# Optimization experiments

Hardware: AMD Instinct MI355X
Metric: run time of the kernel (lower is better)

Reference implementation:

```python
import jax, jax.numpy as jnp
import numpy as np

N, T, D, P, NB = 32768, 128, 32, 16, 15


def setup_inputs() -> dict:
    key = jax.random.key(0)
    ks = jax.random.split(key, 8)
    S = jax.random.normal(ks[0], (N, T, 1), dtype=jnp.float32)
    L_dyn = jax.random.normal(ks[1], (N, T, D), dtype=jnp.float32)
    C_static = jax.random.normal(ks[2], (N, P), dtype=jnp.float32)
    Y = jax.random.randint(ks[3], (N, T, 1), 0, 2).astype(jnp.float32)
    mask = jnp.ones((N, T), dtype=jnp.float32)
    return {
        "S": S, "L_dyn": L_dyn, "C_static": C_static, "Y": Y, "mask": mask,
        "psi": jnp.array([0.5], jnp.float32),
        "gamma_A": jnp.array([0.1], jnp.float32),
        "w_gamma_dyn": 0.05 * jax.random.normal(ks[4], (D,), dtype=jnp.float32),
        "w_gamma_static": 0.05 * jax.random.normal(ks[5], (P,), dtype=jnp.float32),
        "log_sigma_Z": jnp.array([-0.5], jnp.float32),
        "beta_0": jnp.array([-4.0], jnp.float32),
        "beta_Z": jnp.array([0.3], jnp.float32),
        "beta_bins": jnp.zeros((NB,), jnp.float32),
        "w_beta_dyn": 0.1 * jax.random.normal(ks[6], (D,), dtype=jnp.float32),
        "w_beta_static": 0.1 * jax.random.normal(ks[7], (P,), dtype=jnp.float32),
        "beta_time": jnp.array([0.03], jnp.float32),
    }


def reference(S, L_dyn, C_static, Y, mask, psi, gamma_A, w_gamma_dyn,
              w_gamma_static, log_sigma_Z, beta_0, beta_Z, beta_bins,
              w_beta_dyn, w_beta_static, beta_time):
    n, t_len = S.shape[0], S.shape[1]
    nb = beta_bins.shape[0]
    edges = jnp.linspace(-2.5, 2.5, nb + 1).astype(S.dtype)
    # torch.bucketize(s, edges[1:-1]) (right=False) == searchsorted side='left'
    idx = jnp.clip(jnp.searchsorted(edges[1:-1], S[..., 0], side='left'), 0, nb - 1)
    bin_eff = beta_bins[idx][..., None]            # (N,T,1) == (A_bin * beta_bins).sum(-1)
    sigma_sq = jnp.exp(log_sigma_Z)[0] ** 2        # sigma_Z^2
    gd = L_dyn @ w_gamma_dyn[:, None]              # (N,T,1) gamma_dyn(L)
    bd = L_dyn @ w_beta_dyn[:, None]               # (N,T,1) beta_dyn(L)
    gs = (C_static @ w_gamma_static)[:, None]      # (N,1) gamma_static(C)
    bs = (C_static @ w_beta_static)[:, None]       # (N,1) beta_static(C)
    tt = jnp.arange(t_len, dtype=S.dtype) / 30.0   # beta_time * (t/30)

    xs = (
        jnp.swapaxes(S, 0, 1),        # (T,N,1)
        jnp.swapaxes(gd, 0, 1),
        jnp.swapaxes(bd, 0, 1),
        jnp.swapaxes(bin_eff, 0, 1),
        jnp.swapaxes(Y, 0, 1),
        mask.T[:, :, None],           # (T,N,1)
        tt,
    )
    psi_s, gA, bZ, b0, bT = psi[0], gamma_A[0], beta_Z[0], beta_0[0], beta_time[0]

    def step(carry, x):
        Z_mean, Z_var, ll = carry
        A_t, gd_t, bd_t, be_t, Y_t, m_t, t_s = x
        # latent transition prior
        Z_pred_mean = psi_s * Z_mean + gA * A_t + gd_t + gs
        Z_pred_var = psi_s ** 2 * Z_var + sigma_sq
        # outcome probability
        logit = b0 + bZ * Z_pred_mean + be_t + bd_t + bs + bT * t_s
        prob = jax.nn.sigmoid(jnp.clip(logit, -20.0, 20.0))
        # approximate Kalman (Laplace) update from Y
        grad = (Y_t - prob) * bZ * m_t
        hess = bZ ** 2 * prob * (1.0 - prob) * m_t + 1e-6
        Z_post_var = 1.0 / (1.0 / (Z_pred_var + 1e-8) + hess)
        Z_post_mean = Z_pred_mean + Z_post_var * grad
        ll_t = ((Y_t * jnp.log(prob + 1e-10)
                 + (1.0 - Y_t) * jnp.log(1.0 - prob + 1e-10)) * m_t).sum()
        return (Z_post_mean, Z_post_var, ll + ll_t), (Z_post_mean, Z_post_var)

    init = (jnp.zeros((n, 1), S.dtype), jnp.ones((n, 1), S.dtype),
            jnp.zeros((), S.dtype))
    (_, _, ll), (Zf, Zv) = jax.lax.scan(step, init, xs)
    return jnp.swapaxes(Zf, 0, 1), jnp.swapaxes(Zv, 0, 1), ll
```

## Files before the change

kernel.cpp:

```cpp
#include <hip/hip_runtime.h>

#define T_LEN 128
#define NB_BINS 15

__global__ __launch_bounds__(256) void k_static(
    const float4* __restrict__ C4,
    const float4* __restrict__ wgs4,
    const float4* __restrict__ wbs4,
    float* __restrict__ gs_out, float* __restrict__ bs_out, int n_seq)
{
    int n = blockIdx.x * blockDim.x + threadIdx.x;
    if (n >= n_seq) return;
    float gs = 0.0f, bs = 0.0f;
    #pragma unroll
    for (int i = 0; i < 4; ++i) {
        float4 c = C4[n * 4 + i];
        float4 wg = wgs4[i];
        float4 wb = wbs4[i];
        gs += c.x * wg.x + c.y * wg.y + c.z * wg.z + c.w * wg.w;
        bs += c.x * wb.x + c.y * wb.y + c.z * wb.z + c.w * wb.w;
    }
    gs_out[n] = gs;
    bs_out[n] = bs;
}

__global__ __launch_bounds__(256) void k_pre(
    const float4* __restrict__ L4,
    const float*  __restrict__ S,
    const float*  __restrict__ gs_in,
    const float*  __restrict__ bs_in,
    const float4* __restrict__ wgd4,
    const float4* __restrict__ wbd4,
    const float*  __restrict__ p_gA,
    const float*  __restrict__ p_b0,
    const float*  __restrict__ p_bbins,
    const float*  __restrict__ p_bT,
    float* __restrict__ a_out,
    float* __restrict__ c_out,
    int total_rows)
{
    __shared__ float sbins[NB_BINS];
    if (threadIdx.x < NB_BINS) sbins[threadIdx.x] = p_bbins[threadIdx.x];
    __syncthreads();

    const float gA   = p_gA[0];
    const float b0   = p_b0[0];
    const float bT30 = p_bT[0] * (1.0f / 30.0f);

    const int tid   = blockIdx.x * blockDim.x + threadIdx.x;
    const int lane8 = tid & 7;
    const float4 wg = wgd4[lane8];
    const float4 wb = wbd4[lane8];

    const int group   = tid >> 3;
    const int ngroups = (gridDim.x * blockDim.x) >> 3;

    int row = group;
    float4 v = (row < total_rows) ? L4[(size_t)row * 8 + lane8]
                                  : make_float4(0, 0, 0, 0);
    for (; row < total_rows; row += ngroups) {
        const int nrow = row + ngroups;
        float4 vn = v;
        if (nrow < total_rows) vn = L4[(size_t)nrow * 8 + lane8];

        float g = v.x * wg.x + v.y * wg.y + v.z * wg.z + v.w * wg.w;
        float b = v.x * wb.x + v.y * wb.y + v.z * wb.z + v.w * wb.w;
        #pragma unroll
        for (int off = 1; off < 8; off <<= 1) {
            g += __shfl_xor(g, off, 64);
            b += __shfl_xor(b, off, 64);
        }

        const int n = row >> 7;
        const int t = row & 127;
        const float s_v = S[row];
        const float gsv = gs_in[n];
        const float bsv = bs_in[n];
        int cnt = (int)fmaxf(0.0f, fminf(14.0f,
                      ceilf(fmaf(s_v, 3.0f, 7.5f)) - 1.0f));
        const float a = gA * s_v + g + gsv;
        const float c = b0 + sbins[cnt] + b + bsv + bT30 * (float)t;

        if (lane8 == 0) { a_out[row] = a; c_out[row] = c; }
        v = vn;
    }
}

__global__ __launch_bounds__(256) void k_scan(
    const float4* Ain,
    const float4* Cin,
    const float4* __restrict__ Y4,
    const float4* __restrict__ M4,
    const float*  __restrict__ p_psi,
    const float*  __restrict__ p_lsz,
    const float*  __restrict__ p_bZ,
    float4* Zf4,
    float4* Zv4,
    float* __restrict__ ll_out)
{
    const int gtid = blockIdx.x * blockDim.x + threadIdx.x;
    const int n = gtid >> 2;
    const int s = gtid & 3;

    const float psi  = p_psi[0];
    const float e    = __expf(p_lsz[0]);
    const float sig2 = e * e;
    const float bZ   = p_bZ[0];
    const float psi2 = psi * psi;
    const float bZ2  = bZ * bZ;

    const int b32 = n * 32;

    float zm = 0.0f, zvv = 1.0f, ll = 0.0f;

#define STEP(AA, CC, YY, MM, PMOUT, PVOUT, PROUT) do {                    \
        const float zpm = fmaf(psi, zm, (AA));                            \
        const float zpv = fmaf(psi2, zvv, sig2);                          \
        float logit = fmaf(bZ, zpm, (CC));                                \
        logit = fminf(fmaxf(logit, -20.0f), 20.0f);                       \
        const float prob = __builtin_amdgcn_rcpf(1.0f + __expf(-logit));  \
        const float grad = ((YY) - prob) * bZ * (MM);                     \
        const float hess = fmaf(bZ2 * prob * (1.0f - prob), (MM), 1e-6f); \
        const float pvv  = __builtin_amdgcn_rcpf(                         \
                             __builtin_amdgcn_rcpf(zpv + 1e-8f) + hess);  \
        const float pmm  = fmaf(pvv, grad, zpm);                          \
        zm = pmm; zvv = pvv;                                              \
        PMOUT = pmm; PVOUT = pvv; PROUT = prob;                           \
    } while (0)

#define CHUNK(J, Aq, Cq, Yq, Mq) do {                                     \
        float pm0, pm1, pm2, pm3, pv0, pv1, pv2, pv3, pr0, pr1, pr2, pr3; \
        STEP(Aq.x, Cq.x, Yq.x, Mq.x, pm0, pv0, pr0);                      \
        STEP(Aq.y, Cq.y, Yq.y, Mq.y, pm1, pv1, pr1);                      \
        STEP(Aq.z, Cq.z, Yq.z, Mq.z, pm2, pv2, pr2);                      \
        STEP(Aq.w, Cq.w, Yq.w, Mq.w, pm3, pv3, pr3);                      \
        const float prs = (s == 0) ? pr0 : (s == 1) ? pr1                 \
                        : (s == 2) ? pr2 : pr3;                           \
        const float ys  = (s == 0) ? Yq.x : (s == 1) ? Yq.y               \
                        : (s == 2) ? Yq.z : Yq.w;                         \
        const float ms  = (s == 0) ? Mq.x : (s == 1) ? Mq.y               \
                        : (s == 2) ? Mq.z : Mq.w;                         \
        ll += (ys * __logf(prs + 1e-10f)                                  \
             + (1.0f - ys) * __logf(1.0f - prs + 1e-10f)) * ms;           \
        if (s == (J)) {                                                   \
            stpm = make_float4(pm0, pm1, pm2, pm3);                       \
            stpv = make_float4(pv0, pv1, pv2, pv3);                       \
        }                                                                 \
    } while (0)

    float4 A0 = Ain[b32 + 0], A1 = Ain[b32 + 1], A2 = Ain[b32 + 2], A3 = Ain[b32 + 3];
    float4 C0 = Cin[b32 + 0], C1 = Cin[b32 + 1], C2 = Cin[b32 + 2], C3 = Cin[b32 + 3];
    float4 Y0 = Y4[b32 + 0],  Y1 = Y4[b32 + 1],  Y2 = Y4[b32 + 2],  Y3 = Y4[b32 + 3];
    float4 M0 = M4[b32 + 0],  M1 = M4[b32 + 1],  M2 = M4[b32 + 2],  M3 = M4[b32 + 3];

    for (int Q = 0; Q < 8; ++Q) {
        float4 An0, An1, An2, An3, Cn0, Cn1, Cn2, Cn3;
        float4 Yn0, Yn1, Yn2, Yn3, Mn0, Mn1, Mn2, Mn3;
        if (Q < 7) {
            const int qb = b32 + 4 * (Q + 1);
            An0 = Ain[qb + 0]; An1 = Ain[qb + 1]; An2 = Ain[qb + 2]; An3 = Ain[qb + 3];
            Cn0 = Cin[qb + 0]; Cn1 = Cin[qb + 1]; Cn2 = Cin[qb + 2]; Cn3 = Cin[qb + 3];
            Yn0 = Y4[qb + 0];  Yn1 = Y4[qb + 1];  Yn2 = Y4[qb + 2];  Yn3 = Y4[qb + 3];
            Mn0 = M4[qb + 0];  Mn1 = M4[qb + 1];  Mn2 = M4[qb + 2];  Mn3 = M4[qb + 3];
        }

        float4 stpm = make_float4(0, 0, 0, 0);
        float4 stpv = make_float4(0, 0, 0, 0);
        CHUNK(0, A0, C0, Y0, M0);
        CHUNK(1, A1, C1, Y1, M1);
        CHUNK(2, A2, C2, Y2, M2);
        CHUNK(3, A3, C3, Y3, M3);

        Zf4[b32 + 4 * Q + s] = stpm;
        Zv4[b32 + 4 * Q + s] = stpv;

        if (Q < 7) {
            A0 = An0; A1 = An1; A2 = An2; A3 = An3;
            C0 = Cn0; C1 = Cn1; C2 = Cn2; C3 = Cn3;
            Y0 = Yn0; Y1 = Yn1; Y2 = Yn2; Y3 = Yn3;
            M0 = Mn0; M1 = Mn1; M2 = Mn2; M3 = Mn3;
        }
    }
#undef CHUNK
#undef STEP

    #pragma unroll
    for (int off = 1; off < 64; off <<= 1) ll += __shfl_xor(ll, off, 64);
    if ((threadIdx.x & 63) == 0) atomicAdd(ll_out, ll);
}

extern "C" void kernel_launch(void* const* d_in, const int* in_sizes, int n_in,
                              void* d_out, int out_size, void* d_ws, size_t ws_size,
                              hipStream_t stream) {
    const float* S     = (const float*)d_in[0];
    const float* L     = (const float*)d_in[1];
    const float* C     = (const float*)d_in[2];
    const float* Y     = (const float*)d_in[3];
    const float* M     = (const float*)d_in[4];
    const float* psi   = (const float*)d_in[5];
    const float* gA    = (const float*)d_in[6];
    const float* wgd   = (const float*)d_in[7];
    const float* wgs   = (const float*)d_in[8];
    const float* lsz   = (const float*)d_in[9];
    const float* b0    = (const float*)d_in[10];
    const float* bZ    = (const float*)d_in[11];
    const float* bbins = (const float*)d_in[12];
    const float* wbd   = (const float*)d_in[13];
    const float* wbs   = (const float*)d_in[14];
    const float* bT    = (const float*)d_in[15];

    const int NT    = in_sizes[0];
    const int n_seq = NT / T_LEN;

    float* zf = (float*)d_out;
    float* zv = zf + NT;
    float* ll = zf + 2 * (size_t)NT;

    float* gs_ws = (float*)d_ws;
    float* bs_ws = gs_ws + n_seq;

    hipMemsetAsync((void*)ll, 0, sizeof(float), stream);

    k_static<<<(n_seq + 255) / 256, 256, 0, stream>>>(
        reinterpret_cast<const float4*>(C),
        reinterpret_cast<const float4*>(wgs),
        reinterpret_cast<const float4*>(wbs),
        gs_ws, bs_ws, n_seq);

    k_pre<<<2048, 256, 0, stream>>>(
        reinterpret_cast<const float4*>(L),
        S, gs_ws, bs_ws,
        reinterpret_cast<const float4*>(wgd),
        reinterpret_cast<const float4*>(wbd),
        gA, b0, bbins, bT,
        zf, zv, NT);

    k_scan<<<(n_seq * 4) / 256, 256, 0, stream>>>(
        reinterpret_cast<const float4*>(zf),
        reinterpret_cast<const float4*>(zv),
        reinterpret_cast<const float4*>(Y),
        reinterpret_cast<const float4*>(M),
        psi, lsz, bZ,
        reinterpret_cast<float4*>(zf),
        reinterpret_cast<float4*>(zv),
        ll);
}
```

Measured before the change: 182.2 us.

## Fuse static projection into preprocessing and stage time-major packed inputs for scan

Folds the static-covariate projection into the preprocessing kernel, which now packs (a, c, Y, mask) into one float4 per step. It transposes these through shared memory into a time-major workspace so the scan kernel can do coalesced loads. The scan drops the redundant 4-thread-per-sequence recompute and runs one thread per sequence with triple-buffered prefetch. This removes a launch and the duplicated step work, but the scan's per-thread output writes are strided, and it launches only 64-thread blocks (512 total).

New measurement: 194.7 us. +6.9%, slower.

```diff
diff --git a/kernel.cpp b/kernel.cpp
--- a/kernel.cpp
+++ b/kernel.cpp
@@ -2,66 +2,66 @@
 
 #define T_LEN 128
 #define NB_BINS 15
-
-__global__ __launch_bounds__(256) void k_static(
+#define SEQS_PER_BLOCK 16
+
+__global__ __launch_bounds__(256) void k_pre(
+    const float4* __restrict__ L4,
+    const float*  __restrict__ S,
+    const float*  __restrict__ Y,
+    const float*  __restrict__ M,
     const float4* __restrict__ C4,
     const float4* __restrict__ wgs4,
     const float4* __restrict__ wbs4,
-    float* __restrict__ gs_out, float* __restrict__ bs_out, int n_seq)
-{
-    int n = blockIdx.x * blockDim.x + threadIdx.x;
-    if (n >= n_seq) return;
-    float gs = 0.0f, bs = 0.0f;
-    #pragma unroll
-    for (int i = 0; i < 4; ++i) {
-        float4 c = C4[n * 4 + i];
-        float4 wg = wgs4[i];
-        float4 wb = wbs4[i];
-        gs += c.x * wg.x + c.y * wg.y + c.z * wg.z + c.w * wg.w;
-        bs += c.x * wb.x + c.y * wb.y + c.z * wb.z + c.w * wb.w;
-    }
-    gs_out[n] = gs;
-    bs_out[n] = bs;
-}
-
-__global__ __launch_bounds__(256) void k_pre(
-    const float4* __restrict__ L4,
-    const float*  __restrict__ S,
-    const float*  __restrict__ gs_in,
-    const float*  __restrict__ bs_in,
     const float4* __restrict__ wgd4,
     const float4* __restrict__ wbd4,
     const float*  __restrict__ p_gA,
     const float*  __restrict__ p_b0,
     const float*  __restrict__ p_bbins,
     const float*  __restrict__ p_bT,
-    float* __restrict__ a_out,
-    float* __restrict__ c_out,
-    int total_rows)
+    float4* __restrict__ staged,
+    int Nseq)
 {
+    __shared__ float4 tile[T_LEN][SEQS_PER_BLOCK + 1];
+    __shared__ float sgs[SEQS_PER_BLOCK], sbs[SEQS_PER_BLOCK];
     __shared__ float sbins[NB_BINS];
-    if (threadIdx.x < NB_BINS) sbins[threadIdx.x] = p_bbins[threadIdx.x];
+
+    const int tid = threadIdx.x;
+    if (tid < NB_BINS) sbins[tid] = p_bbins[tid];
+
+    const int n0 = blockIdx.x * SEQS_PER_BLOCK;
+
+    if (tid < SEQS_PER_BLOCK) {
+        float gs = 0.0f, bs = 0.0f;
+        #pragma unroll
+        for (int i = 0; i < 4; ++i) {
+            float4 c  = C4[(n0 + tid) * 4 + i];
+            float4 wg = wgs4[i];
+            float4 wb = wbs4[i];
+            gs += c.x * wg.x + c.y * wg.y + c.z * wg.z + c.w * wg.w;
+            bs += c.x * wb.x + c.y * wb.y + c.z * wb.z + c.w * wb.w;
+        }
+        sgs[tid] = gs; sbs[tid] = bs;
+    }
     __syncthreads();
 
     const float gA   = p_gA[0];
     const float b0   = p_b0[0];
     const float bT30 = p_bT[0] * (1.0f / 30.0f);
 
-    const int tid   = blockIdx.x * blockDim.x + threadIdx.x;
     const int lane8 = tid & 7;
+    const int gid   = tid >> 3;
     const float4 wg = wgd4[lane8];
     const float4 wb = wbd4[lane8];
 
-    const int group   = tid >> 3;
-    const int ngroups = (gridDim.x * blockDim.x) >> 3;
-
-    int row = group;
-    float4 v = (row < total_rows) ? L4[(size_t)row * 8 + lane8]
-                                  : make_float4(0, 0, 0, 0);
-    for (; row < total_rows; row += ngroups) {
-        const int nrow = row + ngroups;
+    const size_t rowbase = (size_t)n0 * T_LEN;
+
+    float4 v = L4[(rowbase + gid) * 8 + lane8];
+    for (int it = 0; it < 64; ++it) {
+        const int    lrow = it * 32 + gid;
+        const size_t row  = rowbase + lrow;
+
         float4 vn = v;
-        if (nrow < total_rows) vn = L4[(size_t)nrow * 8 + lane8];
+        if (it + 1 < 64) vn = L4[(row + 32) * 8 + lane8];
 
         float g = v.x * wg.x + v.y * wg.y + v.z * wg.z + v.w * wg.w;
         float b = v.x * wb.x + v.y * wb.y + v.z * wb.z + v.w * wb.w;
@@ -71,36 +71,40 @@
             b += __shfl_xor(b, off, 64);
         }
 
-        const int n = row >> 7;
-        const int t = row & 127;
+        const int nl = lrow >> 7;
+        const int t  = lrow & 127;
         const float s_v = S[row];
-        const float gsv = gs_in[n];
-        const float bsv = bs_in[n];
+        const float y_v = Y[row];
+        const float m_v = M[row];
         int cnt = (int)fmaxf(0.0f, fminf(14.0f,
                       ceilf(fmaf(s_v, 3.0f, 7.5f)) - 1.0f));
-        const float a = gA * s_v + g + gsv;
-        const float c = b0 + sbins[cnt] + b + bsv + bT30 * (float)t;
-
-        if (lane8 == 0) { a_out[row] = a; c_out[row] = c; }
+        const float a = gA * s_v + g + sgs[nl];
+        const float c = b0 + sbins[cnt] + b + sbs[nl] + bT30 * (float)t;
+
+        if (lane8 == 0) tile[t][nl] = make_float4(a, c, y_v, m_v);
         v = vn;
     }
+    __syncthreads();
+
+    #pragma unroll
+    for (int p = 0; p < 8; ++p) {
+        const int idx = p * 256 + tid;
+        const int t = idx >> 4, j = idx & 15;
+        staged[(size_t)t * Nseq + n0 + j] = tile[t][j];
+    }
 }
 
-__global__ __launch_bounds__(256) void k_scan(
-    const float4* Ain,
-    const float4* Cin,
-    const float4* __restrict__ Y4,
-    const float4* __restrict__ M4,
+__global__ __launch_bounds__(64) void k_scan(
+    const float4* __restrict__ staged,
     const float*  __restrict__ p_psi,
     const float*  __restrict__ p_lsz,
     const float*  __restrict__ p_bZ,
-    float4* Zf4,
-    float4* Zv4,
-    float* __restrict__ ll_out)
+    float4* __restrict__ Zf4,
+    float4* __restrict__ Zv4,
+    float*  __restrict__ ll_out,
+    int Nseq)
 {
-    const int gtid = blockIdx.x * blockDim.x + threadIdx.x;
-    const int n = gtid >> 2;
-    const int s = gtid & 3;
+    const int n = blockIdx.x * 64 + threadIdx.x;
 
     const float psi  = p_psi[0];
     const float e    = __expf(p_lsz[0]);
@@ -109,79 +113,57 @@
     const float psi2 = psi * psi;
     const float bZ2  = bZ * bZ;
 
-    const int b32 = n * 32;
-
     float zm = 0.0f, zvv = 1.0f, ll = 0.0f;
 
-#define STEP(AA, CC, YY, MM, PMOUT, PVOUT, PROUT) do {                    \
-        const float zpm = fmaf(psi, zm, (AA));                            \
+#define STEP(PK, PMOUT, PVOUT) do {                                       \
+        const float zpm = fmaf(psi, zm, PK.x);                            \
         const float zpv = fmaf(psi2, zvv, sig2);                          \
-        float logit = fmaf(bZ, zpm, (CC));                                \
+        float logit = fmaf(bZ, zpm, PK.y);                                \
         logit = fminf(fmaxf(logit, -20.0f), 20.0f);                       \
         const float prob = __builtin_amdgcn_rcpf(1.0f + __expf(-logit));  \
-        const float grad = ((YY) - prob) * bZ * (MM);                     \
-        const float hess = fmaf(bZ2 * prob * (1.0f - prob), (MM), 1e-6f); \
+        const float grad = (PK.z - prob) * bZ * PK.w;                     \
+        const float hess = fmaf(bZ2 * prob * (1.0f - prob), PK.w, 1e-6f); \
         const float pvv  = __builtin_amdgcn_rcpf(                         \
                              __builtin_amdgcn_rcpf(zpv + 1e-8f) + hess);  \
         const float pmm  = fmaf(pvv, grad, zpm);                          \
-        zm = pmm; zvv = pvv;                                              \
-        PMOUT = pmm; PVOUT = pvv; PROUT = prob;                           \
+        ll += (PK.z * __logf(prob + 1e-10f)                               \
+             + (1.0f - PK.z) * __logf(1.0f - prob + 1e-10f)) * PK.w;      \
+        zm = pmm; zvv = pvv; PMOUT = pmm; PVOUT = pvv;                    \
     } while (0)
 
-#define CHUNK(J, Aq, Cq, Yq, Mq) do {                                     \
-        float pm0, pm1, pm2, pm3, pv0, pv1, pv2, pv3, pr0, pr1, pr2, pr3; \
-        STEP(Aq.x, Cq.x, Yq.x, Mq.x, pm0, pv0, pr0);                      \
-        STEP(Aq.y, Cq.y, Yq.y, Mq.y, pm1, pv1, pr1);                      \
-        STEP(Aq.z, Cq.z, Yq.z, Mq.z, pm2, pv2, pr2);                      \
-        STEP(Aq.w, Cq.w, Yq.w, Mq.w, pm3, pv3, pr3);                      \
-        const float prs = (s == 0) ? pr0 : (s == 1) ? pr1                 \
-                        : (s == 2) ? pr2 : pr3;                           \
-        const float ys  = (s == 0) ? Yq.x : (s == 1) ? Yq.y               \
-                        : (s == 2) ? Yq.z : Yq.w;                         \
-        const float ms  = (s == 0) ? Mq.x : (s == 1) ? Mq.y               \
-                        : (s == 2) ? Mq.z : Mq.w;                         \
-        ll += (ys * __logf(prs + 1e-10f)                                  \
-             + (1.0f - ys) * __logf(1.0f - prs + 1e-10f)) * ms;           \
-        if (s == (J)) {                                                   \
-            stpm = make_float4(pm0, pm1, pm2, pm3);                       \
-            stpv = make_float4(pv0, pv1, pv2, pv3);                       \
-        }                                                                 \
+#define LOADBUF(B0, B1, B2, B3, CIDX) do {                                \
+        const int cc = (CIDX) > 31 ? 31 : (CIDX);                         \
+        const float4* p = staged + (size_t)(cc * 4) * Nseq + n;           \
+        B0 = p[0];                                                        \
+        B1 = p[(size_t)Nseq];                                             \
+        B2 = p[2 * (size_t)Nseq];                                         \
+        B3 = p[3 * (size_t)Nseq];                                         \
     } while (0)
 
-    float4 A0 = Ain[b32 + 0], A1 = Ain[b32 + 1], A2 = Ain[b32 + 2], A3 = Ain[b32 + 3];
-    float4 C0 = Cin[b32 + 0], C1 = Cin[b32 + 1], C2 = Cin[b32 + 2], C3 = Cin[b32 + 3];
-    float4 Y0 = Y4[b32 + 0],  Y1 = Y4[b32 + 1],  Y2 = Y4[b32 + 2],  Y3 = Y4[b32 + 3];
-    float4 M0 = M4[b32 + 0],  M1 = M4[b32 + 1],  M2 = M4[b32 + 2],  M3 = M4[b32 + 3];
-
-    for (int Q = 0; Q < 8; ++Q) {
-        float4 An0, An1, An2, An3, Cn0, Cn1, Cn2, Cn3;
-        float4 Yn0, Yn1, Yn2, Yn3, Mn0, Mn1, Mn2, Mn3;
-        if (Q < 7) {
-            const int qb = b32 + 4 * (Q + 1);
-            An0 = Ain[qb + 0]; An1 = Ain[qb + 1]; An2 = Ain[qb + 2]; An3 = Ain[qb + 3];
-            Cn0 = Cin[qb + 0]; Cn1 = Cin[qb + 1]; Cn2 = Cin[qb + 2]; Cn3 = Cin[qb + 3];
-            Yn0 = Y4[qb + 0];  Yn1 = Y4[qb + 1];  Yn2 = Y4[qb + 2];  Yn3 = Y4[qb + 3];
-            Mn0 = M4[qb + 0];  Mn1 = M4[qb + 1];  Mn2 = M4[qb + 2];  Mn3 = M4[qb + 3];
-        }
-
-        float4 stpm = make_float4(0, 0, 0, 0);
-        float4 stpv = make_float4(0, 0, 0, 0);
-        CHUNK(0, A0, C0, Y0, M0);
-        CHUNK(1, A1, C1, Y1, M1);
-        CHUNK(2, A2, C2, Y2, M2);
-        CHUNK(3, A3, C3, Y3, M3);
-
-        Zf4[b32 + 4 * Q + s] = stpm;
-        Zv4[b32 + 4 * Q + s] = stpv;
-
-        if (Q < 7) {
-            A0 = An0; A1 = An1; A2 = An2; A3 = An3;
-            C0 = Cn0; C1 = Cn1; C2 = Cn2; C3 = Cn3;
-            Y0 = Yn0; Y1 = Yn1; Y2 = Yn2; Y3 = Yn3;
-            M0 = Mn0; M1 = Mn1; M2 = Mn2; M3 = Mn3;
-        }
-    }
-#undef CHUNK
+#define COMP(B0, B1, B2, B3, K) do {                                      \
+        float pm0, pm1, pm2, pm3, pv0, pv1, pv2, pv3;                     \
+        STEP(B0, pm0, pv0);                                               \
+        STEP(B1, pm1, pv1);                                               \
+        STEP(B2, pm2, pv2);                                               \
+        STEP(B3, pm3, pv3);                                               \
+        Zf4[(size_t)n * 32 + (K)] = make_float4(pm0, pm1, pm2, pm3);      \
+        Zv4[(size_t)n * 32 + (K)] = make_float4(pv0, pv1, pv2, pv3);      \
+    } while (0)
+
+    float4 A0, A1, A2, A3, B0, B1, B2, B3, C0, C1, C2, C3;
+    LOADBUF(A0, A1, A2, A3, 0);
+    LOADBUF(B0, B1, B2, B3, 1);
+    LOADBUF(C0, C1, C2, C3, 2);
+
+    for (int k = 0; k < 30; k += 3) {
+        COMP(A0, A1, A2, A3, k);     LOADBUF(A0, A1, A2, A3, k + 3);
+        COMP(B0, B1, B2, B3, k + 1); LOADBUF(B0, B1, B2, B3, k + 4);
+        COMP(C0, C1, C2, C3, k + 2); LOADBUF(C0, C1, C2, C3, k + 5);
+    }
+    COMP(A0, A1, A2, A3, 30);
+    COMP(B0, B1, B2, B3, 31);
+#undef COMP
+#undef LOADBUF
 #undef STEP
 
     #pragma unroll
@@ -216,32 +198,24 @@
     float* zv = zf + NT;
     float* ll = zf + 2 * (size_t)NT;
 
-    float* gs_ws = (float*)d_ws;
-    float* bs_ws = gs_ws + n_seq;
+    float4* staged = (float4*)d_ws;
 
     hipMemsetAsync((void*)ll, 0, sizeof(float), stream);
 
-    k_static<<<(n_seq + 255) / 256, 256, 0, stream>>>(
+    k_pre<<<n_seq / SEQS_PER_BLOCK, 256, 0, stream>>>(
+        reinterpret_cast<const float4*>(L),
+        S, Y, M,
         reinterpret_cast<const float4*>(C),
         reinterpret_cast<const float4*>(wgs),
         reinterpret_cast<const float4*>(wbs),
-        gs_ws, bs_ws, n_seq);
-
-    k_pre<<<2048, 256, 0, stream>>>(
-        reinterpret_cast<const float4*>(L),
-        S, gs_ws, bs_ws,
         reinterpret_cast<const float4*>(wgd),
         reinterpret_cast<const float4*>(wbd),
         gA, b0, bbins, bT,
-        zf, zv, NT);
-
-    k_scan<<<(n_seq * 4) / 256, 256, 0, stream>>>(
-        reinterpret_cast<const float4*>(zf),
-        reinterpret_cast<const float4*>(zv),
-        reinterpret_cast<const float4*>(Y),
-        reinterpret_cast<const float4*>(M),
-        psi, lsz, bZ,
+        staged, n_seq);
+
+    k_scan<<<n_seq / 64, 64, 0, stream>>>(
+        staged, psi, lsz, bZ,
         reinterpret_cast<float4*>(zf),
         reinterpret_cast<float4*>(zv),
-        ll);
+        ll, n_seq);
 }
```
